# Optimization experiments

Measured on AMD Instinct MI355X. Metric: run time of the kernel, lower is better.

The kernel has to match this reference:

```python
import jax, jax.numpy as jnp
import numpy as np

N_NODES = 50000
N_EDGES = 800000
IN_DIM, HID, N_CLS = 128, 128, 64


def setup_inputs() -> dict:
    key = jax.random.key(0)
    ks = jax.random.split(key, 10)
    x = jax.random.normal(ks[0], (N_NODES, IN_DIM), dtype=jnp.float32)
    src = jax.random.randint(ks[1], (N_EDGES,), 0, N_NODES, dtype=jnp.int32)
    dst = jax.random.randint(ks[2], (N_EDGES,), 0, N_NODES, dtype=jnp.int32)
    def lin(k, fi, fo):
        s = 1.0 / np.sqrt(fi)
        return jax.random.uniform(k, (fi, fo), jnp.float32, -s, s)
    # layer dims: 128->128, 128->128, 128->64 (num_layers=2 -> 3 SAGEConv layers)
    params = {
        'W_self0': lin(ks[3], IN_DIM, HID), 'W_neigh0': lin(ks[4], IN_DIM, HID),
        'b0': jnp.zeros((HID,), jnp.float32),
        'W_self1': lin(ks[5], HID, HID), 'W_neigh1': lin(ks[6], HID, HID),
        'b1': jnp.zeros((HID,), jnp.float32),
        'W_self2': lin(ks[7], HID, N_CLS), 'W_neigh2': lin(ks[8], HID, N_CLS),
        'b2': jnp.zeros((N_CLS,), jnp.float32),
    }
    return {'x': x, 'src': src, 'dst': dst, **params}


def _sage_layer(h, src, dst, W_self, W_neigh, b):
    # mean aggregator: gather source features, segment-sum into dst, divide by in-degree
    msg = h[src]                                                   # [E, d]
    agg = jax.ops.segment_sum(msg, dst, num_segments=N_NODES)      # [N, d]
    deg = jax.ops.segment_sum(jnp.ones((src.shape[0],), h.dtype), dst,
                              num_segments=N_NODES)
    h_neigh = agg / jnp.maximum(deg, 1.0)[:, None]
    return h @ W_self + h_neigh @ W_neigh + b


def reference(x, src, dst, W_self0, W_neigh0, b0, W_self1, W_neigh1, b1,
              W_self2, W_neigh2, b2):
    h = _sage_layer(x, src, dst, W_self0, W_neigh0, b0)
    h = jax.nn.relu(h)
    h = _sage_layer(h, src, dst, W_self1, W_neigh1, b1)
    h = jax.nn.relu(h)
    h = _sage_layer(h, src, dst, W_self2, W_neigh2, b2)
    return h
```

## Files before the change

### kernel.cpp

```cpp
#include <hip/hip_runtime.h>
#include <hip/hip_bf16.h>


#define NFEAT 128
#define SLOTS 64

typedef __attribute__((ext_vector_type(8))) short short8;
typedef __attribute__((ext_vector_type(4))) float floatx4;

__device__ __forceinline__ float bf_lo(unsigned u) { return __uint_as_float(u << 16); }
__device__ __forceinline__ float bf_hi(unsigned u) { return __uint_as_float(u & 0xffff0000u); }
__device__ __forceinline__ ushort f2bf(float f) {
    __hip_bfloat16 h = __float2bfloat16(f);
    return *(ushort*)&h;
}
__device__ __forceinline__ unsigned pack2(float a, float b) {
    return (unsigned)f2bf(a) | ((unsigned)f2bf(b) << 16);
}


__global__ __launch_bounds__(256) void k_prep(
    const int* __restrict__ dst, const int* __restrict__ src,
    int* __restrict__ deg, int* __restrict__ csr,
    int E, int NN,
    const float* __restrict__ X, ushort* __restrict__ X16, int n2,
    const float* __restrict__ Ws0, const float* __restrict__ Wn0,
    const float* __restrict__ Ws1, const float* __restrict__ Wn1,
    const float* __restrict__ Ws2, const float* __restrict__ Wn2,
    ushort* __restrict__ Wt0, ushort* __restrict__ Wt1, ushort* __restrict__ Wt2,
    int e8b, int cvtb) {
    int b = blockIdx.x, t = threadIdx.x;
    if (b < e8b) {
        int base = (b * 256 + t) * 8;
        if (base + 8 <= E) {
            int4 da = *(const int4*)(dst + base);
            int4 db = *(const int4*)(dst + base + 4);
            int4 sa = *(const int4*)(src + base);
            int4 sb = *(const int4*)(src + base + 4);
            int r0 = atomicAdd(&deg[da.x], 1);
            int r1 = atomicAdd(&deg[da.y], 1);
            int r2 = atomicAdd(&deg[da.z], 1);
            int r3 = atomicAdd(&deg[da.w], 1);
            int r4 = atomicAdd(&deg[db.x], 1);
            int r5 = atomicAdd(&deg[db.y], 1);
            int r6 = atomicAdd(&deg[db.z], 1);
            int r7 = atomicAdd(&deg[db.w], 1);
            if (r0 < SLOTS) csr[(da.x << 6) + r0] = sa.x;
            if (r1 < SLOTS) csr[(da.y << 6) + r1] = sa.y;
            if (r2 < SLOTS) csr[(da.z << 6) + r2] = sa.z;
            if (r3 < SLOTS) csr[(da.w << 6) + r3] = sa.w;
            if (r4 < SLOTS) csr[(db.x << 6) + r4] = sb.x;
            if (r5 < SLOTS) csr[(db.y << 6) + r5] = sb.y;
            if (r6 < SLOTS) csr[(db.z << 6) + r6] = sb.z;
            if (r7 < SLOTS) csr[(db.w << 6) + r7] = sb.w;
        } else {
            for (int e = base; e < E; ++e) {
                int d = dst[e];
                int r = atomicAdd(&deg[d], 1);
                if (r < SLOTS) csr[(d << 6) + r] = src[e];
            }
        }
    } else if (b < e8b + cvtb) {
        int i = (b - e8b) * 256 + t;
        if (i < n2) {
            float2 v = ((const float2*)X)[i];
            ((unsigned*)X16)[i] = pack2(v.x, v.y);
        }
    } else {
        int idx = (b - e8b - cvtb) * 256 + t;
        if (idx < 32768) {
            int n = idx >> 8, k = idx & 255;
            Wt0[idx] = f2bf(k < 128 ? Ws0[k * 128 + n] : Wn0[(k - 128) * 128 + n]);
        } else if (idx < 65536) {
            int l = idx - 32768, n = l >> 8, k = l & 255;
            Wt1[l] = f2bf(k < 128 ? Ws1[k * 128 + n] : Wn1[(k - 128) * 128 + n]);
        } else if (idx < 81920) {
            int l = idx - 65536, n = l >> 8, k = l & 255;
            Wt2[l] = f2bf(k < 128 ? Ws2[k * 64 + n] : Wn2[(k - 128) * 64 + n]);
        }
    }
}


template <int FEAT, int MODE>
__device__ __forceinline__ void agg_body(int vbid, int nb, int t,
    const ushort* __restrict__ H, const int* __restrict__ deg,
    const int* __restrict__ csr, void* __restrict__ outp, int NN) {
    constexpr int LPR = FEAT / 8;
    constexpr int EPG = 64 / LPR;
    constexpr int NS = 8;
    int lane = t & 63, wid = t >> 6;
    int sub = lane / LPR, fl = lane % LPR;
    int wstr = nb * 4;
    int node = vbid * 4 + wid;

    int d_cur = 0;
    int s_cur[NS];
    if (node < NN) {
        d_cur = deg[node];
        const int* slot = csr + (node << 6);
#pragma unroll
        for (int k = 0; k < NS; ++k) s_cur[k] = slot[k * EPG + sub];
    }

    while (node < NN) {
        int nnode = node + wstr;
        int d_nxt = 0;
        int s_nxt[NS];
        if (nnode < NN) {
            d_nxt = deg[nnode];
            const int* slot2 = csr + (nnode << 6);
#pragma unroll
            for (int k = 0; k < NS; ++k) s_nxt[k] = slot2[k * EPG + sub];
        }

        int dd = d_cur;
        int d = (dd < SLOTS) ? dd : SLOTS;
        float acc[8] = {};
        uint4 v[NS];
#pragma unroll
        for (int k = 0; k < NS; ++k) {
            int e = k * EPG + sub;
            v[k] = make_uint4(0, 0, 0, 0);
            if (e < d) v[k] = *(const uint4*)(H + (size_t)s_cur[k] * FEAT + fl * 8);
        }
#pragma unroll
        for (int k = 0; k < NS; ++k) {
            acc[0] += bf_lo(v[k].x); acc[1] += bf_hi(v[k].x);
            acc[2] += bf_lo(v[k].y); acc[3] += bf_hi(v[k].y);
            acc[4] += bf_lo(v[k].z); acc[5] += bf_hi(v[k].z);
            acc[6] += bf_lo(v[k].w); acc[7] += bf_hi(v[k].w);
        }
        if constexpr (NS * EPG < SLOTS) {
            if (d > NS * EPG) {
                const int* slot = csr + (node << 6);
                for (int e = NS * EPG + sub; e < d; e += EPG) {
                    int r = slot[e];
                    uint4 vv = *(const uint4*)(H + (size_t)r * FEAT + fl * 8);
                    acc[0] += bf_lo(vv.x); acc[1] += bf_hi(vv.x);
                    acc[2] += bf_lo(vv.y); acc[3] += bf_hi(vv.y);
                    acc[4] += bf_lo(vv.z); acc[5] += bf_hi(vv.z);
                    acc[6] += bf_lo(vv.w); acc[7] += bf_hi(vv.w);
                }
            }
        }
#pragma unroll
        for (int off = LPR; off < 64; off <<= 1)
#pragma unroll
            for (int i = 0; i < 8; ++i) acc[i] += __shfl_xor(acc[i], off, 64);
        if (sub == 0) {
            float inv = (dd > 0) ? 1.0f / (float)dd : 0.0f;
            if constexpr (MODE == 0) {
                unsigned u[4];
#pragma unroll
                for (int i = 0; i < 4; ++i)
                    u[i] = pack2(acc[2 * i] * inv, acc[2 * i + 1] * inv);
                *(uint4*)((ushort*)outp + (size_t)node * FEAT + fl * 8) =
                    make_uint4(u[0], u[1], u[2], u[3]);
            } else {
                float* O = (float*)outp;
                size_t b = (size_t)node * FEAT + fl * 8;
#pragma unroll
                for (int i = 0; i < 8; ++i) O[b + i] += acc[i] * inv;
            }
        }
        node = nnode;
        d_cur = d_nxt;
#pragma unroll
        for (int k = 0; k < NS; ++k) s_cur[k] = s_nxt[k];
    }
}

__global__ __launch_bounds__(256) void k_agg128(
    const ushort* __restrict__ H, const int* __restrict__ deg,
    const int* __restrict__ csr, void* __restrict__ outp, int NN) {
    agg_body<128, 0>(blockIdx.x, gridDim.x, threadIdx.x, H, deg, csr, outp, NN);
}

__global__ __launch_bounds__(256) void k_aggacc(
    const ushort* __restrict__ G2, const int* __restrict__ deg,
    const int* __restrict__ csr, float* __restrict__ out, int NN) {
    agg_body<64, 2>(blockIdx.x, gridDim.x, threadIdx.x, G2, deg, csr, out, NN);
}


template <int BM, int BN, int NKB, bool SPLIT, bool OUT_BF16>
__device__ __forceinline__ void gemm_body(int bid, int t,
    const ushort* __restrict__ Hs, const ushort* __restrict__ Ag,
    const ushort* __restrict__ Wt, int ldw, const float* __restrict__ bias,
    void* __restrict__ Cout, int M, int relu) {
    constexpr int NW = BN / 64;
    constexpr int NTHR = 2 * NW * 64;
    constexpr int MT = BM / 32;
    constexpr int LDA = 40;
    __shared__ ushort Asl[BM * LDA];
    __shared__ ushort Bsl[BN * LDA];

    int lane = t & 63;
    int wid = t >> 6;
    int wm = wid & 1, wn = wid >> 1;
    int l15 = lane & 15, quad = lane >> 4;
    int m0 = bid * BM;

    floatx4 acc[MT][4] = {};

    for (int kb = 0; kb < NKB; ++kb) {
        const ushort* Asrc;
        int kOff;
        if constexpr (SPLIT) {
            Asrc = (kb < NKB / 2) ? Hs : Ag;
            kOff = (kb & (NKB / 2 - 1)) * 32;
        } else {
            Asrc = Hs;
            kOff = kb * 32;
        }
        __syncthreads();
#pragma unroll
        for (int id = t; id < BM * 4; id += NTHR) {
            int r = id >> 2, p = id & 3;
            uint4 v = make_uint4(0, 0, 0, 0);
            if (m0 + r < M) v = *(const uint4*)(Asrc + (size_t)(m0 + r) * NFEAT + kOff + p * 8);
            *(uint4*)(&Asl[r * LDA + p * 8]) = v;
        }
#pragma unroll
        for (int id = t; id < BN * 4; id += NTHR) {
            int r = id >> 2, p = id & 3;
            uint4 v = *(const uint4*)(Wt + (size_t)r * ldw + kb * 32 + p * 8);
            *(uint4*)(&Bsl[r * LDA + p * 8]) = v;
        }
        __syncthreads();

        short8 a[MT], b[4];
#pragma unroll
        for (int mt = 0; mt < MT; ++mt)
            a[mt] = *(const short8*)(&Asl[(wm * (MT * 16) + mt * 16 + l15) * LDA + quad * 8]);
#pragma unroll
        for (int nt = 0; nt < 4; ++nt)
            b[nt] = *(const short8*)(&Bsl[(wn * 64 + nt * 16 + l15) * LDA + quad * 8]);
#pragma unroll
        for (int mt = 0; mt < MT; ++mt)
#pragma unroll
            for (int nt = 0; nt < 4; ++nt)
                acc[mt][nt] = __builtin_amdgcn_mfma_f32_16x16x32_bf16(a[mt], b[nt], acc[mt][nt], 0, 0, 0);
    }

#pragma unroll
    for (int mt = 0; mt < MT; ++mt) {
        int mbase = m0 + wm * (MT * 16) + mt * 16 + quad * 4;
#pragma unroll
        for (int nt = 0; nt < 4; ++nt) {
            int col = wn * 64 + nt * 16 + l15;
            float bv = bias ? bias[col] : 0.0f;
#pragma unroll
            for (int r = 0; r < 4; ++r) {
                int m = mbase + r;
                if (m < M) {
                    float v = acc[mt][nt][r] + bv;
                    if (relu) v = fmaxf(v, 0.f);
                    if constexpr (OUT_BF16) {
                        ((unsigned short*)Cout)[(size_t)m * BN + col] = f2bf(v);
                    } else {
                        ((float*)Cout)[(size_t)m * BN + col] = v;
                    }
                }
            }
        }
    }
}

__global__ __launch_bounds__(256) void k_gemm(
    const ushort* __restrict__ Hs, const ushort* __restrict__ Ag,
    const ushort* __restrict__ Wt, const float* __restrict__ bias,
    ushort* __restrict__ Hout, int M) {
    gemm_body<64, 128, 8, true, true>(blockIdx.x, threadIdx.x,
                                      Hs, Ag, Wt, 256, bias, Hout, M, 1);
}

__global__ __launch_bounds__(128) void k_d7(
    const ushort* __restrict__ Hb, const ushort* __restrict__ Wt2,
    const float* __restrict__ b2, ushort* __restrict__ G2,
    float* __restrict__ out, int M, int pb) {
    if ((int)blockIdx.x < pb)
        gemm_body<64, 64, 4, false, true>(blockIdx.x, threadIdx.x,
                                          Hb, nullptr, Wt2 + 128, 256, nullptr, G2, M, 0);
    else
        gemm_body<64, 64, 4, false, false>(blockIdx.x - pb, threadIdx.x,
                                           Hb, nullptr, Wt2, 256, b2, out, M, 0);
}


static inline size_t align_up(size_t x) { return (x + 255) & ~(size_t)255; }

extern "C" void kernel_launch(void* const* d_in, const int* in_sizes, int n_in,
                              void* d_out, int out_size, void* d_ws, size_t ws_size,
                              hipStream_t stream) {
    const float* x   = (const float*)d_in[0];
    const int*   src = (const int*)d_in[1];
    const int*   dst = (const int*)d_in[2];
    const float* Ws0 = (const float*)d_in[3];
    const float* Wn0 = (const float*)d_in[4];
    const float* b0  = (const float*)d_in[5];
    const float* Ws1 = (const float*)d_in[6];
    const float* Wn1 = (const float*)d_in[7];
    const float* b1  = (const float*)d_in[8];
    const float* Ws2 = (const float*)d_in[9];
    const float* Wn2 = (const float*)d_in[10];
    const float* b2  = (const float*)d_in[11];
    float* out = (float*)d_out;

    const int NN = in_sizes[0] / NFEAT;
    const int E  = in_sizes[1];

    char* w = (char*)d_ws;
    ushort* X16  = (ushort*)w; w += align_up((size_t)NN * NFEAT * 2);
    ushort* Ha   = (ushort*)w; w += align_up((size_t)NN * NFEAT * 2);
    ushort* Hb   = (ushort*)w; w += align_up((size_t)NN * NFEAT * 2);
    ushort* AGG  = (ushort*)w; w += align_up((size_t)NN * NFEAT * 2);
    ushort* Wt0  = (ushort*)w; w += align_up((size_t)128 * 256 * 2);
    ushort* Wt1  = (ushort*)w; w += align_up((size_t)128 * 256 * 2);
    ushort* Wt2  = (ushort*)w; w += align_up((size_t)64 * 256 * 2);
    int* deg     = (int*)w;    w += align_up((size_t)NN * 4);
    int* csr     = (int*)w;    w += align_up((size_t)NN * SLOTS * 4);

    ushort* G2  = X16;

    hipMemsetAsync(deg, 0, (size_t)NN * 4, stream);

    const int e8b  = (E / 8 + 255) / 256;
    const int n2   = NN * NFEAT / 2;
    const int cvtb = (n2 + 255) / 256;
    const int wb   = (81920 + 255) / 256;
    const int gm   = (NN + 63) / 64;
    const int agb  = 2048;

    k_prep<<<e8b + cvtb + wb, 256, 0, stream>>>(
        dst, src, deg, csr, E, NN, x, X16, n2,
        Ws0, Wn0, Ws1, Wn1, Ws2, Wn2, Wt0, Wt1, Wt2, e8b, cvtb);

    k_agg128<<<agb, 256, 0, stream>>>(X16, deg, csr, AGG, NN);
    k_gemm<<<gm, 256, 0, stream>>>(X16, AGG, Wt0, b0, Ha, NN);

    k_agg128<<<agb, 256, 0, stream>>>(Ha, deg, csr, AGG, NN);
    k_gemm<<<gm, 256, 0, stream>>>(Ha, AGG, Wt1, b1, Hb, NN);

    k_d7<<<gm * 2, 128, 0, stream>>>(Hb, Wt2, b2, G2, out, NN, gm);
    k_aggacc<<<agb, 256, 0, stream>>>(G2, deg, csr, out, NN);
}
```

Before: 265.7 us.

## Partition CSR build by XCC with per-XCC work queues and workgroup-scope atomics

The edge-bucketing phase now has each wavefront read its XCC id and pull 512-edge chunks from a per-XCC atomic counter. Each XCC processes only the destination nodes whose (d>>4)&7 matches its id, so atomics on a given deg entry stay within one XCC's L2 and can use workgroup scope instead of device scope. The cost is that every XCC reads the full edge list, and correctness depends on workgroup-scope atomics being coherent across all CUs of one XCC. It also assumes all 8 XCCs host some of the 1024 edge blocks; any XCC without a resident block would leave its partition unprocessed.

```diff
diff --git a/kernel.cpp b/kernel.cpp
--- a/kernel.cpp
+++ b/kernel.cpp
@@ -18,56 +18,70 @@
     return (unsigned)f2bf(a) | ((unsigned)f2bf(b) << 16);
 }
 
+__device__ __forceinline__ int xcc_id() {
+    int x;
+    asm volatile("s_getreg_b32 %0, hwreg(HW_REG_XCC_ID)" : "=s"(x));
+    return x & 7;
+}
+
+
+__device__ __forceinline__ void edge_one(int d, int s, int myx,
+                                         int* __restrict__ deg,
+                                         int* __restrict__ csr) {
+    if (((d >> 4) & 7) != myx) return;
+    int r = __hip_atomic_fetch_add(&deg[d], 1, __ATOMIC_RELAXED,
+                                   __HIP_MEMORY_SCOPE_WORKGROUP);
+    if (r < SLOTS) csr[(d << 6) + r] = s;
+}
 
 __global__ __launch_bounds__(256) void k_prep(
     const int* __restrict__ dst, const int* __restrict__ src,
-    int* __restrict__ deg, int* __restrict__ csr,
+    int* __restrict__ deg, int* __restrict__ csr, int* __restrict__ wq,
     int E, int NN,
     const float* __restrict__ X, ushort* __restrict__ X16, int n2,
     const float* __restrict__ Ws0, const float* __restrict__ Wn0,
     const float* __restrict__ Ws1, const float* __restrict__ Wn1,
     const float* __restrict__ Ws2, const float* __restrict__ Wn2,
     ushort* __restrict__ Wt0, ushort* __restrict__ Wt1, ushort* __restrict__ Wt2,
-    int e8b, int cvtb) {
+    int eb, int cvtb) {
     int b = blockIdx.x, t = threadIdx.x;
-    if (b < e8b) {
-        int base = (b * 256 + t) * 8;
-        if (base + 8 <= E) {
-            int4 da = *(const int4*)(dst + base);
-            int4 db = *(const int4*)(dst + base + 4);
-            int4 sa = *(const int4*)(src + base);
-            int4 sb = *(const int4*)(src + base + 4);
-            int r0 = atomicAdd(&deg[da.x], 1);
-            int r1 = atomicAdd(&deg[da.y], 1);
-            int r2 = atomicAdd(&deg[da.z], 1);
-            int r3 = atomicAdd(&deg[da.w], 1);
-            int r4 = atomicAdd(&deg[db.x], 1);
-            int r5 = atomicAdd(&deg[db.y], 1);
-            int r6 = atomicAdd(&deg[db.z], 1);
-            int r7 = atomicAdd(&deg[db.w], 1);
-            if (r0 < SLOTS) csr[(da.x << 6) + r0] = sa.x;
-            if (r1 < SLOTS) csr[(da.y << 6) + r1] = sa.y;
-            if (r2 < SLOTS) csr[(da.z << 6) + r2] = sa.z;
-            if (r3 < SLOTS) csr[(da.w << 6) + r3] = sa.w;
-            if (r4 < SLOTS) csr[(db.x << 6) + r4] = sb.x;
-            if (r5 < SLOTS) csr[(db.y << 6) + r5] = sb.y;
-            if (r6 < SLOTS) csr[(db.z << 6) + r6] = sb.z;
-            if (r7 < SLOTS) csr[(db.w << 6) + r7] = sb.w;
-        } else {
-            for (int e = base; e < E; ++e) {
-                int d = dst[e];
-                int r = atomicAdd(&deg[d], 1);
-                if (r < SLOTS) csr[(d << 6) + r] = src[e];
+    if (b < eb) {
+        int lane = t & 63;
+        int myx = xcc_id();
+        int* cnt = wq + myx;
+        const int nch = (E + 511) >> 9;
+        for (;;) {
+            int ck = 0;
+            if (lane == 0) ck = atomicAdd(cnt, 1);
+            ck = __shfl(ck, 0, 64);
+            if (ck >= nch) break;
+            int base = (ck << 9) + lane * 8;
+            if (base + 8 <= E) {
+                int4 da = *(const int4*)(dst + base);
+                int4 db = *(const int4*)(dst + base + 4);
+                int4 sa = *(const int4*)(src + base);
+                int4 sb = *(const int4*)(src + base + 4);
+                edge_one(da.x, sa.x, myx, deg, csr);
+                edge_one(da.y, sa.y, myx, deg, csr);
+                edge_one(da.z, sa.z, myx, deg, csr);
+                edge_one(da.w, sa.w, myx, deg, csr);
+                edge_one(db.x, sb.x, myx, deg, csr);
+                edge_one(db.y, sb.y, myx, deg, csr);
+                edge_one(db.z, sb.z, myx, deg, csr);
+                edge_one(db.w, sb.w, myx, deg, csr);
+            } else {
+                for (int e = base; e < E && e < base + 8; ++e)
+                    edge_one(dst[e], src[e], myx, deg, csr);
             }
         }
-    } else if (b < e8b + cvtb) {
-        int i = (b - e8b) * 256 + t;
+    } else if (b < eb + cvtb) {
+        int i = (b - eb) * 256 + t;
         if (i < n2) {
             float2 v = ((const float2*)X)[i];
             ((unsigned*)X16)[i] = pack2(v.x, v.y);
         }
     } else {
-        int idx = (b - e8b - cvtb) * 256 + t;
+        int idx = (b - eb - cvtb) * 256 + t;
         if (idx < 32768) {
             int n = idx >> 8, k = idx & 255;
             Wt0[idx] = f2bf(k < 128 ? Ws0[k * 128 + n] : Wn0[(k - 128) * 128 + n]);
@@ -319,23 +333,24 @@
     ushort* Wt0  = (ushort*)w; w += align_up((size_t)128 * 256 * 2);
     ushort* Wt1  = (ushort*)w; w += align_up((size_t)128 * 256 * 2);
     ushort* Wt2  = (ushort*)w; w += align_up((size_t)64 * 256 * 2);
-    int* deg     = (int*)w;    w += align_up((size_t)NN * 4);
+    int* deg     = (int*)w;    w += align_up((size_t)(NN + 16) * 4);
     int* csr     = (int*)w;    w += align_up((size_t)NN * SLOTS * 4);
 
     ushort* G2  = X16;
-
-    hipMemsetAsync(deg, 0, (size_t)NN * 4, stream);
-
-    const int e8b  = (E / 8 + 255) / 256;
+    int* wq     = deg + NN;
+
+    hipMemsetAsync(deg, 0, (size_t)(NN + 16) * 4, stream);
+
+    const int eb   = 1024;
     const int n2   = NN * NFEAT / 2;
     const int cvtb = (n2 + 255) / 256;
     const int wb   = (81920 + 255) / 256;
     const int gm   = (NN + 63) / 64;
     const int agb  = 2048;
 
-    k_prep<<<e8b + cvtb + wb, 256, 0, stream>>>(
-        dst, src, deg, csr, E, NN, x, X16, n2,
-        Ws0, Wn0, Ws1, Wn1, Ws2, Wn2, Wt0, Wt1, Wt2, e8b, cvtb);
+    k_prep<<<eb + cvtb + wb, 256, 0, stream>>>(
+        dst, src, deg, csr, wq, E, NN, x, X16, n2,
+        Ws0, Wn0, Ws1, Wn1, Ws2, Wn2, Wt0, Wt1, Wt2, eb, cvtb);
 
     k_agg128<<<agb, 256, 0, stream>>>(X16, deg, csr, AGG, NN);
     k_gemm<<<gm, 256, 0, stream>>>(X16, AGG, Wt0, b0, Ha, NN);
```

Result: slower. 422.5 us (+59.0%).
